# Kernel optimization log

Measured on AMD Instinct MI355X. Metric: run time of the kernel, lower is better.

Reference implementation:

```python
import jax, jax.numpy as jnp
import numpy as np

N_NODES = 100000
IN_FEATS = 256
N_EDGES = 3200000
N_SEL = 4096
J_POOL = 50  # eval branch: inner loop over first 50 selected nodes


def setup_inputs() -> dict:
    key = jax.random.key(0)
    ks = jax.random.split(key, 16)
    x = jax.random.normal(ks[0], (N_NODES, IN_FEATS), dtype=jnp.float32)
    edge_index = jax.random.randint(ks[1], (2, N_EDGES), 0, N_NODES)
    nodes = jax.random.randint(ks[2], (N_SEL,), 0, N_NODES)
    s1 = 1.0 / np.sqrt(IN_FEATS)
    s2 = 1.0 / np.sqrt(32)
    s3 = 1.0 / np.sqrt(16)
    return {
        "x": x,
        "w1": jax.random.uniform(ks[3], (IN_FEATS, 32), jnp.float32, -s1, s1),
        "b1": jnp.zeros((32,), jnp.float32),
        "w2": jax.random.uniform(ks[4], (32, 16), jnp.float32, -s2, s2),
        "b2": jnp.zeros((16,), jnp.float32),
        "gate1_w": jax.random.normal(ks[5], (32, 4), jnp.float32) * 0.02,
        "e1_w": jax.random.uniform(ks[6], (4, 32, 16), jnp.float32, -s2, s2),
        "e1_b": jnp.zeros((4, 16), jnp.float32),
        "gate2_w": jax.random.normal(ks[7], (16, 4), jnp.float32) * 0.02,
        "e2_w": jax.random.uniform(ks[8], (4, 16, 2), jnp.float32, -s3, s3),
        "e2_b": jnp.zeros((4, 2), jnp.float32),
        "edge_index": edge_index,
        "nodes": nodes,
    }


def _gcn_conv(h, w, b, src, dst, n):
    hw = h @ w
    deg = jnp.zeros((n,), hw.dtype).at[dst].add(1.0)
    dis = jax.lax.rsqrt(jnp.maximum(deg, 1e-12))
    norm = dis[src] * dis[dst]
    msg = hw[src] * norm[:, None]
    return jax.ops.segment_sum(msg, dst, num_segments=n) + b


def _moe_top1(z, gate_w, ew, eb):
    # k=1 gating: softmax over a single selected logit == weight 1.0
    idx = jnp.argmax(z @ gate_w, axis=-1)              # [M]
    outs = jnp.einsum('mi,eio->meo', z, ew) + eb        # [M, E, O]
    return jnp.take_along_axis(outs, idx[:, None, None], axis=1)[:, 0]


def reference(x, w1, b1, w2, b2, gate1_w, e1_w, e1_b, gate2_w, e2_w, e2_b,
              edge_index, nodes):
    n = x.shape[0]
    loops = jnp.arange(n)
    src = jnp.concatenate([edge_index[0], loops])
    dst = jnp.concatenate([edge_index[1], loops])

    h = jax.nn.relu(_gcn_conv(x, w1, b1, src, dst, n))   # dropout: eval mode (identity)
    h = _gcn_conv(h, w2, b2, src, dst, n)                # [N, 16]

    # eval branch pairwise concat: i over all selected nodes, j over first 50
    hi = jnp.repeat(h[nodes], J_POOL, axis=0)            # [M, 16]
    hj = jnp.tile(h[nodes[:J_POOL]], (nodes.shape[0], 1))  # [M, 16]
    x_sim = jnp.concatenate([hi, hj], axis=-1)           # [M, 32]

    z = jax.nn.relu(_moe_top1(x_sim, gate1_w, e1_w, e1_b))
    z = _moe_top1(z, gate2_w, e2_w, e2_b)                # [M, 2]
    return jax.nn.log_softmax(z, axis=1), x_sim
```

## Files before the change

### kernel.cpp

```cpp
#include <hip/hip_runtime.h>
#include <hip/hip_fp16.h>
#include <math.h>


#define NPB 64
#define NB_PAD 2048
#define BATCH 8192
#define NSCAP 12288

__global__ void zero_kernel(int* __restrict__ p, int c) {
    int i = blockIdx.x * 256 + threadIdx.x;
    if (i < c) p[i] = 0;
}

__global__ __launch_bounds__(256) void histA_kernel(const int* __restrict__ ei,
                                                    int* __restrict__ bhist, int nE, int nb) {
    __shared__ int h[NB_PAD];
    int tid = threadIdx.x;
    for (int t = tid; t < nb; t += 256) h[t] = 0;
    __syncthreads();
    int base = blockIdx.x * 4096;
    for (int t = tid; t < 4096; t += 256) {
        int e = base + t;
        if (e < nE) atomicAdd(&h[ei[nE + e] >> 6], 1);
    }
    __syncthreads();
    for (int t = tid; t < nb; t += 256) { int c = h[t]; if (c) atomicAdd(&bhist[t], c); }
}

__global__ __launch_bounds__(256) void scanB_kernel(const int* __restrict__ bhist,
                                                    int* __restrict__ boffs,
                                                    int* __restrict__ gcur, int nb) {
    int t = threadIdx.x;
    int v[8], s = 0;
    #pragma unroll
    for (int i = 0; i < 8; ++i) { int c = t * 8 + i; v[i] = (c < nb) ? bhist[c] : 0; s += v[i]; }
    int lane = t & 63, wid = t >> 6;
    int incl = s;
    for (int d = 1; d < 64; d <<= 1) { int u = __shfl_up(incl, (unsigned)d, 64); if (lane >= d) incl += u; }
    __shared__ int ws[4];
    if (lane == 63) ws[wid] = incl;
    __syncthreads();
    int add = 0;
    for (int w = 0; w < wid; ++w) add += ws[w];
    incl += add;
    int excl = incl - s;
    #pragma unroll
    for (int i = 0; i < 8; ++i) {
        int c = t * 8 + i;
        if (c < nb) { boffs[c] = excl; gcur[c] = excl; }
        excl += v[i];
    }
    if (t == 0) boffs[nb] = ws[0] + ws[1] + ws[2] + ws[3];
}

__global__ __launch_bounds__(256) void scatterC_kernel(const int* __restrict__ ei,
                                                       int* __restrict__ gcur,
                                                       int* __restrict__ keys, int nE, int nb) {
    __shared__ int kbuf[BATCH];
    __shared__ unsigned short kbk[BATCH];
    __shared__ int lstart[NB_PAD];
    __shared__ int cursor[NB_PAD];
    __shared__ int gbase[NB_PAD];
    __shared__ int ws2[4];
    int tid = threadIdx.x;
    int base = blockIdx.x * BATCH;
    int cnt = nE - base; if (cnt > BATCH) cnt = BATCH;
    for (int t = tid; t < nb; t += 256) lstart[t] = 0;
    __syncthreads();
    for (int t = tid; t < cnt; t += 256)
        atomicAdd(&lstart[ei[nE + base + t] >> 6], 1);
    __syncthreads();
    {
        int v[8], s = 0;
        #pragma unroll
        for (int i = 0; i < 8; ++i) { int c = tid * 8 + i; v[i] = (c < nb) ? lstart[c] : 0; s += v[i]; }
        int lane = tid & 63, wid = tid >> 6;
        int incl = s;
        for (int d = 1; d < 64; d <<= 1) { int u = __shfl_up(incl, (unsigned)d, 64); if (lane >= d) incl += u; }
        if (lane == 63) ws2[wid] = incl;
        __syncthreads();
        int add = 0;
        for (int w = 0; w < wid; ++w) add += ws2[w];
        incl += add;
        int excl = incl - s;
        #pragma unroll
        for (int i = 0; i < 8; ++i) {
            int c = tid * 8 + i;
            if (c < nb) { lstart[c] = excl; cursor[c] = excl; }
            excl += v[i];
        }
    }
    __syncthreads();
    for (int t = tid; t < nb; t += 256) {
        int e = (t == nb - 1) ? cnt : lstart[t + 1];
        int c = e - lstart[t];
        gbase[t] = c ? atomicAdd(&gcur[t], c) : 0;
    }
    for (int t = tid; t < cnt; t += 256) {
        int d = ei[nE + base + t];
        int s = ei[base + t];
        int b = d >> 6;
        int pos = atomicAdd(&cursor[b], 1);
        kbuf[pos] = s | ((d & 63) << 17);
        kbk[pos] = (unsigned short)b;
    }
    __syncthreads();
    for (int j = tid; j < cnt; j += 256) {
        int b = kbk[j];
        keys[gbase[b] + (j - lstart[b])] = kbuf[j];
    }
}

__global__ __launch_bounds__(256) void nodesort_kernel(int* __restrict__ keys,
                                                       const int* __restrict__ boffs,
                                                       int* __restrict__ noffs,
                                                       float* __restrict__ dis,
                                                       int n, int nbuck) {
    __shared__ int kb[NSCAP];
    __shared__ int cnt[NPB], cur[NPB];
    int tid = threadIdx.x, b = blockIdx.x;
    int off = boffs[b], end = boffs[b + 1];
    int m = end - off; if (m > NSCAP) m = NSCAP;
    if (tid < NPB) cnt[tid] = 0;
    __syncthreads();
    for (int t = tid; t < m; t += 256) {
        int k = keys[off + t];
        kb[t] = k;
        atomicAdd(&cnt[k >> 17], 1);
    }
    __syncthreads();
    if (tid < NPB) {
        int v = cnt[tid];
        int incl = v;
        for (int d = 1; d < 64; d <<= 1) { int u = __shfl_up(incl, (unsigned)d, 64); if (tid >= d) incl += u; }
        int excl = incl - v;
        cur[tid] = excl;
        int node = b * NPB + tid;
        if (node < n) {
            noffs[node] = off + excl;
            dis[node] = rsqrtf((float)(v + 1));
        }
    }
    __syncthreads();
    for (int t = tid; t < m; t += 256) {
        int k = kb[t];
        int pos = atomicAdd(&cur[k >> 17], 1);
        keys[off + pos] = k & 0x1FFFF;
    }
    if (b == nbuck - 1 && tid == 0) noffs[n] = end;
}

__global__ __launch_bounds__(256) void hw1s_kernel(const float* __restrict__ x,
                                                   const float* __restrict__ w1,
                                                   const float* __restrict__ dis,
                                                   __half* __restrict__ hw1h, int n) {
    __shared__ float xs[128 * 68];
    int tid = threadIdx.x;
    int row0 = blockIdx.x * 128;
    int r = tid & 127;
    int khs = __builtin_amdgcn_readfirstlane((tid >> 7) * 16);
    float acc[16];
    #pragma unroll
    for (int k = 0; k < 16; ++k) acc[k] = 0.f;

    for (int ch = 0; ch < 4; ++ch) {
        int cc0 = ch * 64;
        __syncthreads();
        #pragma unroll
        for (int i = 0; i < 8; ++i) {
            int gid = i * 256 + tid;
            int rr = gid >> 4, c4 = (gid & 15) << 2;
            int row = row0 + rr;
            float4 v = (row < n) ? *(const float4*)&x[(size_t)row * 256 + cc0 + c4]
                                 : make_float4(0.f, 0.f, 0.f, 0.f);
            *(float4*)&xs[rr * 68 + c4] = v;
        }
        __syncthreads();
        #pragma unroll 4
        for (int cg = 0; cg < 16; ++cg) {
            float4 xv = *(float4*)&xs[r * 68 + cg * 4];
            const float* wr = &w1[(size_t)(cc0 + cg * 4) * 32 + khs];
            #pragma unroll
            for (int k = 0; k < 16; ++k) acc[k] = fmaf(xv.x, wr[k], acc[k]);
            #pragma unroll
            for (int k = 0; k < 16; ++k) acc[k] = fmaf(xv.y, wr[32 + k], acc[k]);
            #pragma unroll
            for (int k = 0; k < 16; ++k) acc[k] = fmaf(xv.z, wr[64 + k], acc[k]);
            #pragma unroll
            for (int k = 0; k < 16; ++k) acc[k] = fmaf(xv.w, wr[96 + k], acc[k]);
        }
    }
    int row = row0 + r;
    if (row < n) {
        float dn = dis[row];
        __half2 h[8];
        #pragma unroll
        for (int k = 0; k < 8; ++k)
            h[k] = __floats2half2_rn(acc[2 * k] * dn, acc[2 * k + 1] * dn);
        float4* dst = (float4*)&hw1h[(size_t)row * 32 + khs];
        dst[0] = *(float4*)&h[0];
        dst[1] = *(float4*)&h[4];
    }
}

__global__ __launch_bounds__(256) void gatherG1_kernel(const __half* __restrict__ hw1h,
                                                       const float* __restrict__ dis,
                                                       const int* __restrict__ srcs,
                                                       const int* __restrict__ noffs,
                                                       const float* __restrict__ b1,
                                                       __half* __restrict__ h1h, int n) {
    int tid = threadIdx.x;
    int g = tid >> 5, k = tid & 31;
    int node = blockIdx.x * 8 + g;
    if (node >= n) return;
    int off = noffs[node], end = noffs[node + 1];
    float acc = 0.f;
    int e = off;
    for (; e + 8 <= end; e += 8) {
        int s0 = srcs[e],     s1 = srcs[e + 1], s2 = srcs[e + 2], s3 = srcs[e + 3];
        int s4 = srcs[e + 4], s5 = srcs[e + 5], s6 = srcs[e + 6], s7 = srcs[e + 7];
        float v0 = __half2float(hw1h[(size_t)s0 * 32 + k]);
        float v1 = __half2float(hw1h[(size_t)s1 * 32 + k]);
        float v2 = __half2float(hw1h[(size_t)s2 * 32 + k]);
        float v3 = __half2float(hw1h[(size_t)s3 * 32 + k]);
        float v4 = __half2float(hw1h[(size_t)s4 * 32 + k]);
        float v5 = __half2float(hw1h[(size_t)s5 * 32 + k]);
        float v6 = __half2float(hw1h[(size_t)s6 * 32 + k]);
        float v7 = __half2float(hw1h[(size_t)s7 * 32 + k]);
        acc += ((v0 + v1) + (v2 + v3)) + ((v4 + v5) + (v6 + v7));
    }
    for (; e < end; ++e)
        acc += __half2float(hw1h[(size_t)srcs[e] * 32 + k]);
    float dn = dis[node];
    float self = __half2float(hw1h[(size_t)node * 32 + k]);
    float h = fmaxf(dn * (acc + self) + b1[k], 0.f);
    h1h[(size_t)node * 32 + k] = __float2half(h);
}

__global__ __launch_bounds__(256) void gemm2_kernel(const __half* __restrict__ h1h,
                                                    const float* __restrict__ w2,
                                                    const float* __restrict__ dis,
                                                    float* __restrict__ hw2s, int n) {
    __shared__ float w2s[512];
    __shared__ float h1s[16][33];
    int tid = threadIdx.x;
    for (int t = tid; t < 512; t += 256) w2s[t] = w2[t];
    int node0 = blockIdx.x * 16;
    for (int t = tid; t < 512; t += 256) {
        int r = t >> 5, c = t & 31;
        int nd = node0 + r;
        h1s[r][c] = (nd < n) ? __half2float(h1h[(size_t)nd * 32 + c]) : 0.f;
    }
    __syncthreads();
    int r = tid >> 4, j = tid & 15;
    int nd = node0 + r;
    if (nd < n) {
        float a = 0.f;
        #pragma unroll
        for (int c = 0; c < 32; ++c) a += h1s[r][c] * w2s[c * 16 + j];
        hw2s[(size_t)nd * 16 + j] = a * dis[nd];
    }
}

__global__ __launch_bounds__(256) void gatherG2_kernel(const float* __restrict__ hw2s,
                                                       const float* __restrict__ dis,
                                                       const int* __restrict__ srcs,
                                                       const int* __restrict__ noffs,
                                                       const int* __restrict__ nodes,
                                                       const float* __restrict__ b2,
                                                       float* __restrict__ h2, int nsel, int n) {
    int tid = threadIdx.x;
    int slot = tid >> 4, j = tid & 15;
    int i = blockIdx.x * 16 + slot;
    if (i >= nsel) return;
    int node = nodes[i];
    int off = noffs[node], end = noffs[node + 1];
    float acc = 0.f;
    int e = off;
    for (; e + 4 <= end; e += 4) {
        int s0 = srcs[e], s1 = srcs[e + 1], s2 = srcs[e + 2], s3 = srcs[e + 3];
        float v0 = hw2s[(size_t)s0 * 16 + j];
        float v1 = hw2s[(size_t)s1 * 16 + j];
        float v2 = hw2s[(size_t)s2 * 16 + j];
        float v3 = hw2s[(size_t)s3 * 16 + j];
        acc += (v0 + v1) + (v2 + v3);
    }
    for (; e < end; ++e) acc += hw2s[(size_t)srcs[e] * 16 + j];
    h2[(size_t)node * 16 + j] = dis[node] * (acc + hw2s[(size_t)node * 16 + j]) + b2[j];
}

__global__ __launch_bounds__(256) void pair_moe_kernel(const float* __restrict__ h2,
                                                       const int* __restrict__ nodes,
                                                       const float* __restrict__ gate1_w,
                                                       const float* __restrict__ e1_w,
                                                       const float* __restrict__ e1_b,
                                                       const float* __restrict__ gate2_w,
                                                       const float* __restrict__ e2_w,
                                                       const float* __restrict__ e2_b,
                                                       float* __restrict__ out1,
                                                       float* __restrict__ out2, int M) {
    __shared__ float hjs[50 * 16];
    __shared__ float g1s[32 * 4];
    __shared__ float e1ws[4 * 32 * 16];
    __shared__ float e1bs[4 * 16];
    __shared__ float g2s[16 * 4];
    __shared__ float e2ws[4 * 16 * 2];
    __shared__ float e2bs[4 * 2];
    int tid = threadIdx.x;
    for (int t = tid; t < 800; t += 256) { int j = t >> 4, c = t & 15; hjs[t] = h2[nodes[j] * 16 + c]; }
    for (int t = tid; t < 128; t += 256) g1s[t] = gate1_w[t];
    for (int t = tid; t < 2048; t += 256) e1ws[t] = e1_w[t];
    for (int t = tid; t < 64; t += 256) e1bs[t] = e1_b[t];
    for (int t = tid; t < 64; t += 256) g2s[t] = gate2_w[t];
    for (int t = tid; t < 128; t += 256) e2ws[t] = e2_w[t];
    if (tid < 8) e2bs[tid] = e2_b[tid];
    __syncthreads();

    int m = blockIdx.x * 256 + tid;
    if (m >= M) return;
    int i = m / 50, j = m - i * 50;

    float xs[32];
    int ni = nodes[i];
    float4 a0 = *(const float4*)&h2[ni * 16];
    float4 a1 = *(const float4*)&h2[ni * 16 + 4];
    float4 a2 = *(const float4*)&h2[ni * 16 + 8];
    float4 a3 = *(const float4*)&h2[ni * 16 + 12];
    xs[0]=a0.x; xs[1]=a0.y; xs[2]=a0.z; xs[3]=a0.w;
    xs[4]=a1.x; xs[5]=a1.y; xs[6]=a1.z; xs[7]=a1.w;
    xs[8]=a2.x; xs[9]=a2.y; xs[10]=a2.z; xs[11]=a2.w;
    xs[12]=a3.x; xs[13]=a3.y; xs[14]=a3.z; xs[15]=a3.w;
    #pragma unroll
    for (int c = 0; c < 16; ++c) xs[16 + c] = hjs[j * 16 + c];

    #pragma unroll
    for (int c = 0; c < 32; c += 4)
        *(float4*)&out2[(size_t)m * 32 + c] = make_float4(xs[c], xs[c+1], xs[c+2], xs[c+3]);

    float g[4] = {0.f, 0.f, 0.f, 0.f};
    #pragma unroll
    for (int c = 0; c < 32; ++c) {
        float xv = xs[c];
        #pragma unroll
        for (int e = 0; e < 4; ++e) g[e] += xv * g1s[c * 4 + e];
    }
    int idx = 0; float best = g[0];
    #pragma unroll
    for (int e = 1; e < 4; ++e) if (g[e] > best) { best = g[e]; idx = e; }
    float z[16];
    #pragma unroll
    for (int o = 0; o < 16; ++o) {
        float a = e1bs[idx * 16 + o];
        #pragma unroll
        for (int c = 0; c < 32; ++c) a += xs[c] * e1ws[(idx * 32 + c) * 16 + o];
        z[o] = fmaxf(a, 0.f);
    }

    float g2[4] = {0.f, 0.f, 0.f, 0.f};
    #pragma unroll
    for (int c = 0; c < 16; ++c) {
        float zv = z[c];
        #pragma unroll
        for (int e = 0; e < 4; ++e) g2[e] += zv * g2s[c * 4 + e];
    }
    int idx2 = 0; float best2 = g2[0];
    #pragma unroll
    for (int e = 1; e < 4; ++e) if (g2[e] > best2) { best2 = g2[e]; idx2 = e; }
    float z2[2];
    #pragma unroll
    for (int o = 0; o < 2; ++o) {
        float a = e2bs[idx2 * 2 + o];
        #pragma unroll
        for (int c = 0; c < 16; ++c) a += z[c] * e2ws[(idx2 * 16 + c) * 2 + o];
        z2[o] = a;
    }

    float mx = fmaxf(z2[0], z2[1]);
    float l = logf(expf(z2[0] - mx) + expf(z2[1] - mx));
    out1[(size_t)m * 2 + 0] = z2[0] - mx - l;
    out1[(size_t)m * 2 + 1] = z2[1] - mx - l;
}

extern "C" void kernel_launch(void* const* d_in, const int* in_sizes, int n_in,
                              void* d_out, int out_size, void* d_ws, size_t ws_size,
                              hipStream_t stream) {
    const float* x       = (const float*)d_in[0];
    const float* w1      = (const float*)d_in[1];
    const float* b1      = (const float*)d_in[2];
    const float* w2      = (const float*)d_in[3];
    const float* b2      = (const float*)d_in[4];
    const float* gate1_w = (const float*)d_in[5];
    const float* e1_w    = (const float*)d_in[6];
    const float* e1_b    = (const float*)d_in[7];
    const float* gate2_w = (const float*)d_in[8];
    const float* e2_w    = (const float*)d_in[9];
    const float* e2_b    = (const float*)d_in[10];
    const int*   ei      = (const int*)d_in[11];
    const int*   nodes   = (const int*)d_in[12];

    const int n    = in_sizes[0] / 256;
    const int nE   = in_sizes[11] / 2;
    const int nsel = in_sizes[12];
    const int M    = nsel * 50;
    const int nb   = (n + NPB - 1) / NPB;

    size_t off = 0;
    auto alloc = [&](size_t bytes) -> void* {
        void* p = (char*)d_ws + off;
        off += (bytes + 255) & ~(size_t)255;
        return p;
    };
    float*  dis    = (float*)alloc((size_t)n * 4);
    int*    bhist  = (int*)alloc((size_t)nb * 4);
    int*    boffs  = (int*)alloc((size_t)(nb + 1) * 4);
    int*    gcur   = (int*)alloc((size_t)nb * 4);
    int*    noffs  = (int*)alloc((size_t)(n + 1) * 4);
    int*    keys   = (int*)alloc((size_t)nE * 4);
    __half* hw1h   = (__half*)alloc((size_t)n * 32 * 2);
    __half* h1h    = (__half*)alloc((size_t)n * 32 * 2);
    float*  hw2s   = (float*)alloc((size_t)n * 16 * 4);
    float*  h2     = (float*)alloc((size_t)n * 16 * 4);
    if (off > ws_size) return;

    float* out1 = (float*)d_out;
    float* out2 = out1 + (size_t)M * 2;

    zero_kernel<<<(nb + 255) / 256, 256, 0, stream>>>(bhist, nb);
    histA_kernel<<<(nE + 4095) / 4096, 256, 0, stream>>>(ei, bhist, nE, nb);
    scanB_kernel<<<1, 256, 0, stream>>>(bhist, boffs, gcur, nb);
    scatterC_kernel<<<(nE + BATCH - 1) / BATCH, 256, 0, stream>>>(ei, gcur, keys, nE, nb);
    nodesort_kernel<<<nb, 256, 0, stream>>>(keys, boffs, noffs, dis, n, nb);
    hw1s_kernel<<<(n + 127) / 128, 256, 0, stream>>>(x, w1, dis, hw1h, n);
    gatherG1_kernel<<<(n + 7) / 8, 256, 0, stream>>>(hw1h, dis, keys, noffs, b1, h1h, n);
    gemm2_kernel<<<(n + 15) / 16, 256, 0, stream>>>(h1h, w2, dis, hw2s, n);
    gatherG2_kernel<<<(nsel + 15) / 16, 256, 0, stream>>>(hw2s, dis, keys, noffs, nodes, b2,
                                                          h2, nsel, n);
    pair_moe_kernel<<<(M + 255) / 256, 256, 0, stream>>>(h2, nodes, gate1_w, e1_w, e1_b,
                                                         gate2_w, e2_w, e2_b, out1, out2, M);
}
```

Before: 231.8 us.

## Use MFMA f16 for first GEMM and fuse second GEMM into layer-1 gather

The x@w1 projection moves from a shared-memory FP32 FMA loop to wave-level 16x16x32 f16 MFMA instructions. Each wave runs a grid-stride loop over 16-row blocks with w1 fragments held in registers. Separately, the w2 GEMM is fused into the layer-1 gather kernel through shared memory, which removes the h1h intermediate buffer and one kernel launch. The trade-off is that x is rounded to fp16 before the multiply, reducing precision, and the hw1h output stores become narrower and less coalesced.

```diff
diff --git a/kernel.cpp b/kernel.cpp
--- a/kernel.cpp
+++ b/kernel.cpp
@@ -7,6 +7,9 @@
 #define NB_PAD 2048
 #define BATCH 8192
 #define NSCAP 12288
+
+typedef _Float16 half8 __attribute__((ext_vector_type(8)));
+typedef float f32x4 __attribute__((ext_vector_type(4)));
 
 __global__ void zero_kernel(int* __restrict__ p, int c) {
     int i = blockIdx.x * 256 + threadIdx.x;
@@ -155,52 +158,58 @@
                                                    const float* __restrict__ w1,
                                                    const float* __restrict__ dis,
                                                    __half* __restrict__ hw1h, int n) {
-    __shared__ float xs[128 * 68];
-    int tid = threadIdx.x;
-    int row0 = blockIdx.x * 128;
-    int r = tid & 127;
-    int khs = __builtin_amdgcn_readfirstlane((tid >> 7) * 16);
-    float acc[16];
-    #pragma unroll
-    for (int k = 0; k < 16; ++k) acc[k] = 0.f;
-
-    for (int ch = 0; ch < 4; ++ch) {
-        int cc0 = ch * 64;
-        __syncthreads();
-        #pragma unroll
-        for (int i = 0; i < 8; ++i) {
-            int gid = i * 256 + tid;
-            int rr = gid >> 4, c4 = (gid & 15) << 2;
-            int row = row0 + rr;
-            float4 v = (row < n) ? *(const float4*)&x[(size_t)row * 256 + cc0 + c4]
-                                 : make_float4(0.f, 0.f, 0.f, 0.f);
-            *(float4*)&xs[rr * 68 + c4] = v;
-        }
-        __syncthreads();
-        #pragma unroll 4
-        for (int cg = 0; cg < 16; ++cg) {
-            float4 xv = *(float4*)&xs[r * 68 + cg * 4];
-            const float* wr = &w1[(size_t)(cc0 + cg * 4) * 32 + khs];
-            #pragma unroll
-            for (int k = 0; k < 16; ++k) acc[k] = fmaf(xv.x, wr[k], acc[k]);
-            #pragma unroll
-            for (int k = 0; k < 16; ++k) acc[k] = fmaf(xv.y, wr[32 + k], acc[k]);
-            #pragma unroll
-            for (int k = 0; k < 16; ++k) acc[k] = fmaf(xv.z, wr[64 + k], acc[k]);
-            #pragma unroll
-            for (int k = 0; k < 16; ++k) acc[k] = fmaf(xv.w, wr[96 + k], acc[k]);
-        }
-    }
-    int row = row0 + r;
-    if (row < n) {
-        float dn = dis[row];
-        __half2 h[8];
-        #pragma unroll
-        for (int k = 0; k < 8; ++k)
-            h[k] = __floats2half2_rn(acc[2 * k] * dn, acc[2 * k + 1] * dn);
-        float4* dst = (float4*)&hw1h[(size_t)row * 32 + khs];
-        dst[0] = *(float4*)&h[0];
-        dst[1] = *(float4*)&h[4];
+    int tid = threadIdx.x;
+    int lane = tid & 63;
+    int wv = blockIdx.x * 4 + (tid >> 6);
+    int nw = gridDim.x * 4;
+    int mr = lane & 15, grp = lane >> 4;
+
+    half8 bf0[8], bf1[8];
+    #pragma unroll
+    for (int kc = 0; kc < 8; ++kc) {
+        half8 b0, b1v;
+        #pragma unroll
+        for (int e = 0; e < 8; ++e) {
+            int k = kc * 32 + grp * 8 + e;
+            b0[e]  = (_Float16)w1[k * 32 + mr];
+            b1v[e] = (_Float16)w1[k * 32 + 16 + mr];
+        }
+        bf0[kc] = b0; bf1[kc] = b1v;
+    }
+
+    int nblk = (n + 15) >> 4;
+    for (int blk = wv; blk < nblk; blk += nw) {
+        int row = (blk << 4) + mr;
+        int rowc = (row < n) ? row : n - 1;
+        const float* xr = &x[(size_t)rowc * 256 + grp * 8];
+        half8 af[8];
+        #pragma unroll
+        for (int kc = 0; kc < 8; ++kc) {
+            float4 u = *(const float4*)&xr[kc * 32];
+            float4 v = *(const float4*)&xr[kc * 32 + 4];
+            half8 a;
+            a[0] = (_Float16)u.x; a[1] = (_Float16)u.y;
+            a[2] = (_Float16)u.z; a[3] = (_Float16)u.w;
+            a[4] = (_Float16)v.x; a[5] = (_Float16)v.y;
+            a[6] = (_Float16)v.z; a[7] = (_Float16)v.w;
+            af[kc] = a;
+        }
+        f32x4 acc0 = {0.f, 0.f, 0.f, 0.f}, acc1 = {0.f, 0.f, 0.f, 0.f};
+        #pragma unroll
+        for (int kc = 0; kc < 8; ++kc)
+            acc0 = __builtin_amdgcn_mfma_f32_16x16x32_f16(af[kc], bf0[kc], acc0, 0, 0, 0);
+        #pragma unroll
+        for (int kc = 0; kc < 8; ++kc)
+            acc1 = __builtin_amdgcn_mfma_f32_16x16x32_f16(af[kc], bf1[kc], acc1, 0, 0, 0);
+        #pragma unroll
+        for (int i = 0; i < 4; ++i) {
+            int orow = (blk << 4) + grp * 4 + i;
+            if (orow < n) {
+                float dn = dis[orow];
+                hw1h[(size_t)orow * 32 + mr]      = __float2half(acc0[i] * dn);
+                hw1h[(size_t)orow * 32 + 16 + mr] = __float2half(acc1[i] * dn);
+            }
+        }
     }
 }
 
@@ -209,57 +218,49 @@
                                                        const int* __restrict__ srcs,
                                                        const int* __restrict__ noffs,
                                                        const float* __restrict__ b1,
-                                                       __half* __restrict__ h1h, int n) {
-    int tid = threadIdx.x;
+                                                       const float* __restrict__ w2,
+                                                       float* __restrict__ hw2s, int n) {
+    __shared__ float h1s[8][33];
+    __shared__ float w2s[512];
+    int tid = threadIdx.x;
+    for (int t = tid; t < 512; t += 256) w2s[t] = w2[t];
     int g = tid >> 5, k = tid & 31;
     int node = blockIdx.x * 8 + g;
-    if (node >= n) return;
-    int off = noffs[node], end = noffs[node + 1];
-    float acc = 0.f;
-    int e = off;
-    for (; e + 8 <= end; e += 8) {
-        int s0 = srcs[e],     s1 = srcs[e + 1], s2 = srcs[e + 2], s3 = srcs[e + 3];
-        int s4 = srcs[e + 4], s5 = srcs[e + 5], s6 = srcs[e + 6], s7 = srcs[e + 7];
-        float v0 = __half2float(hw1h[(size_t)s0 * 32 + k]);
-        float v1 = __half2float(hw1h[(size_t)s1 * 32 + k]);
-        float v2 = __half2float(hw1h[(size_t)s2 * 32 + k]);
-        float v3 = __half2float(hw1h[(size_t)s3 * 32 + k]);
-        float v4 = __half2float(hw1h[(size_t)s4 * 32 + k]);
-        float v5 = __half2float(hw1h[(size_t)s5 * 32 + k]);
-        float v6 = __half2float(hw1h[(size_t)s6 * 32 + k]);
-        float v7 = __half2float(hw1h[(size_t)s7 * 32 + k]);
-        acc += ((v0 + v1) + (v2 + v3)) + ((v4 + v5) + (v6 + v7));
-    }
-    for (; e < end; ++e)
-        acc += __half2float(hw1h[(size_t)srcs[e] * 32 + k]);
-    float dn = dis[node];
-    float self = __half2float(hw1h[(size_t)node * 32 + k]);
-    float h = fmaxf(dn * (acc + self) + b1[k], 0.f);
-    h1h[(size_t)node * 32 + k] = __float2half(h);
-}
-
-__global__ __launch_bounds__(256) void gemm2_kernel(const __half* __restrict__ h1h,
-                                                    const float* __restrict__ w2,
-                                                    const float* __restrict__ dis,
-                                                    float* __restrict__ hw2s, int n) {
-    __shared__ float w2s[512];
-    __shared__ float h1s[16][33];
-    int tid = threadIdx.x;
-    for (int t = tid; t < 512; t += 256) w2s[t] = w2[t];
-    int node0 = blockIdx.x * 16;
-    for (int t = tid; t < 512; t += 256) {
-        int r = t >> 5, c = t & 31;
-        int nd = node0 + r;
-        h1s[r][c] = (nd < n) ? __half2float(h1h[(size_t)nd * 32 + c]) : 0.f;
-    }
-    __syncthreads();
-    int r = tid >> 4, j = tid & 15;
-    int nd = node0 + r;
-    if (nd < n) {
-        float a = 0.f;
-        #pragma unroll
-        for (int c = 0; c < 32; ++c) a += h1s[r][c] * w2s[c * 16 + j];
-        hw2s[(size_t)nd * 16 + j] = a * dis[nd];
+    float h = 0.f;
+    if (node < n) {
+        int off = noffs[node], end = noffs[node + 1];
+        float acc = 0.f;
+        int e = off;
+        for (; e + 8 <= end; e += 8) {
+            int s0 = srcs[e],     s1 = srcs[e + 1], s2 = srcs[e + 2], s3 = srcs[e + 3];
+            int s4 = srcs[e + 4], s5 = srcs[e + 5], s6 = srcs[e + 6], s7 = srcs[e + 7];
+            float v0 = __half2float(hw1h[(size_t)s0 * 32 + k]);
+            float v1 = __half2float(hw1h[(size_t)s1 * 32 + k]);
+            float v2 = __half2float(hw1h[(size_t)s2 * 32 + k]);
+            float v3 = __half2float(hw1h[(size_t)s3 * 32 + k]);
+            float v4 = __half2float(hw1h[(size_t)s4 * 32 + k]);
+            float v5 = __half2float(hw1h[(size_t)s5 * 32 + k]);
+            float v6 = __half2float(hw1h[(size_t)s6 * 32 + k]);
+            float v7 = __half2float(hw1h[(size_t)s7 * 32 + k]);
+            acc += ((v0 + v1) + (v2 + v3)) + ((v4 + v5) + (v6 + v7));
+        }
+        for (; e < end; ++e)
+            acc += __half2float(hw1h[(size_t)srcs[e] * 32 + k]);
+        float dn = dis[node];
+        float self = __half2float(hw1h[(size_t)node * 32 + k]);
+        h = fmaxf(dn * (acc + self) + b1[k], 0.f);
+    }
+    h1s[g][k] = h;
+    __syncthreads();
+    if (tid < 128) {
+        int gg = tid >> 4, j = tid & 15;
+        int nd = blockIdx.x * 8 + gg;
+        if (nd < n) {
+            float a = 0.f;
+            #pragma unroll
+            for (int c = 0; c < 32; ++c) a += h1s[gg][c] * w2s[c * 16 + j];
+            hw2s[(size_t)nd * 16 + j] = a * dis[nd];
+        }
     }
 }
 
@@ -418,7 +419,6 @@
     int*    noffs  = (int*)alloc((size_t)(n + 1) * 4);
     int*    keys   = (int*)alloc((size_t)nE * 4);
     __half* hw1h   = (__half*)alloc((size_t)n * 32 * 2);
-    __half* h1h    = (__half*)alloc((size_t)n * 32 * 2);
     float*  hw2s   = (float*)alloc((size_t)n * 16 * 4);
     float*  h2     = (float*)alloc((size_t)n * 16 * 4);
     if (off > ws_size) return;
@@ -431,9 +431,8 @@
     scanB_kernel<<<1, 256, 0, stream>>>(bhist, boffs, gcur, nb);
     scatterC_kernel<<<(nE + BATCH - 1) / BATCH, 256, 0, stream>>>(ei, gcur, keys, nE, nb);
     nodesort_kernel<<<nb, 256, 0, stream>>>(keys, boffs, noffs, dis, n, nb);
-    hw1s_kernel<<<(n + 127) / 128, 256, 0, stream>>>(x, w1, dis, hw1h, n);
-    gatherG1_kernel<<<(n + 7) / 8, 256, 0, stream>>>(hw1h, dis, keys, noffs, b1, h1h, n);
-    gemm2_kernel<<<(n + 15) / 16, 256, 0, stream>>>(h1h, w2, dis, hw2s, n);
+    hw1s_kernel<<<768, 256, 0, stream>>>(x, w1, dis, hw1h, n);
+    gatherG1_kernel<<<(n + 7) / 8, 256, 0, stream>>>(hw1h, dis, keys, noffs, b1, w2, hw2s, n);
     gatherG2_kernel<<<(nsel + 15) / 16, 256, 0, stream>>>(hw2s, dis, keys, noffs, nodes, b2,
                                                           h2, nsel, n);
     pair_moe_kernel<<<(M + 255) / 256, 256, 0, stream>>>(h2, nodes, gate1_w, e1_w, e1_b,
```

New measurement: 208.7 us. -10.0%, faster.
